# Optimization experiments

Hardware: AMD Instinct MI355X
Metric: run time of the kernel (lower is better)

## Reference

```python
import jax, jax.numpy as jnp
import numpy as np

B, S, H = 32, 2048, 1024

def setup_inputs() -> dict:
    key = jax.random.key(0)
    ks = jax.random.split(key, 6)
    sc = 0.02
    return {
        "decoder_state": jax.random.normal(ks[0], (B, H), jnp.float32),
        "encoder_output": jax.random.normal(ks[1], (B, S, H), jnp.float32),
        "coverage_vector": jax.random.uniform(ks[2], (B, S), jnp.float32),
        "Wh": jax.random.normal(ks[3], (H, H), jnp.float32) * sc,
        "bh": jnp.zeros((H,), jnp.float32),
        "Ws": jax.random.normal(ks[4], (H, H), jnp.float32) * sc,
        "bs": jnp.zeros((H,), jnp.float32),
        "V": jax.random.normal(ks[5], (H, 1), jnp.float32) * sc,
        "bv": jnp.zeros((1,), jnp.float32),
        "Wc": jax.random.normal(jax.random.fold_in(key, 7), (S, 1), jnp.float32) * sc,
        "bc": jnp.zeros((1,), jnp.float32),
    }

def reference(decoder_state, encoder_output, coverage_vector, Wh, bh, Ws, bs, V, bv, Wc, bc):
    # enc proj: (B,S,H); dec proj broadcast: (B,1,H)
    enc_p = jnp.einsum('bsh,hk->bsk', encoder_output, Wh) + bh
    dec_p = (decoder_state @ Ws + bs)[:, None, :]
    # Faithful to TF code: wc acts on expanded coverage (B,1,S) -> (B,1,1) scalar per batch
    cov_p = (coverage_vector @ Wc + bc)[:, None, :]          # (B,1,1)
    score = jnp.tanh(enc_p + dec_p + cov_p) @ V + bv          # (B,S,1)
    attention_weights = jax.nn.softmax(score, axis=1)        # (B,S,1)
    coverage_new = coverage_vector + attention_weights[..., 0]  # (B,S)
    context_vector = jnp.sum(attention_weights * encoder_output, axis=1)  # (B,H)
    return (context_vector, attention_weights, coverage_new)
```

## Files before the change

kernel.cpp:

```cpp
#include <hip/hip_runtime.h>

#define B_ 32
#define S_ 2048
#define H_ 1024

typedef __attribute__((ext_vector_type(8))) short short8;
typedef __attribute__((ext_vector_type(4))) float f32x4;
typedef __attribute__((ext_vector_type(4))) unsigned short u16x4;

__device__ __forceinline__ unsigned short f2bf(float f) {
    unsigned u = __builtin_bit_cast(unsigned, f);
    u += 0x7FFFu + ((u >> 16) & 1u);
    return (unsigned short)(u >> 16);
}
__device__ __forceinline__ unsigned pk2(float x, float y) {
    return (unsigned)f2bf(x) | ((unsigned)f2bf(y) << 16);
}
__device__ __forceinline__ float bf2f(unsigned short u) {
    unsigned x = ((unsigned)u) << 16;
    return __builtin_bit_cast(float, x);
}
__device__ __forceinline__ void gload16(const void* g, void* l) {
    __builtin_amdgcn_global_load_lds((const __attribute__((address_space(1))) void*)g,
                                     (__attribute__((address_space(3))) void*)l, 16, 0, 0);
}

#define WAITV(nstr) asm volatile("s_waitcnt vmcnt(" nstr ")" ::: "memory")

__global__ void k_cvt(const float* __restrict__ in, uint4* __restrict__ out, int ngroups) {
    int i = blockIdx.x * blockDim.x + threadIdx.x;
    int stride = gridDim.x * blockDim.x;
    for (; i < ngroups; i += stride) {
        const float4* p = (const float4*)in + (size_t)i * 2;
        float4 x = p[0], y = p[1];
        out[i] = make_uint4(pk2(x.x, x.y), pk2(x.z, x.w), pk2(y.x, y.y), pk2(y.z, y.w));
    }
}

__global__ void k_whT(const float* __restrict__ Wh, unsigned short* __restrict__ whT) {
    __shared__ float tile[64][65];
    int k0 = blockIdx.x * 64, n0 = blockIdx.y * 64;
    int tx = threadIdx.x, ty = threadIdx.y;
    #pragma unroll
    for (int i = 0; i < 16; ++i) {
        int r = ty + i * 4;
        tile[r][tx] = Wh[(size_t)(k0 + r) * H_ + n0 + tx];
    }
    __syncthreads();
    #pragma unroll
    for (int i = 0; i < 16; ++i) {
        int r = ty + i * 4;
        whT[(size_t)(n0 + r) * H_ + k0 + tx] = f2bf(tile[tx][r]);
    }
}

__global__ void k_decp(const float* __restrict__ ds, const float* __restrict__ Ws,
                       const float* __restrict__ bs, const float* __restrict__ bh,
                       float* __restrict__ decp) {
    int n = blockIdx.x * 256 + threadIdx.x;
    int b = blockIdx.y;
    float a0 = 0.f, a1 = 0.f, a2 = 0.f, a3 = 0.f;
    for (int h = 0; h < H_; h += 4) {
        a0 += ds[b * H_ + h + 0] * Ws[(size_t)(h + 0) * H_ + n];
        a1 += ds[b * H_ + h + 1] * Ws[(size_t)(h + 1) * H_ + n];
        a2 += ds[b * H_ + h + 2] * Ws[(size_t)(h + 2) * H_ + n];
        a3 += ds[b * H_ + h + 3] * Ws[(size_t)(h + 3) * H_ + n];
    }
    decp[b * H_ + n] = a0 + a1 + a2 + a3 + bs[n] + bh[n];
}

__global__ void k_covp(const float* __restrict__ cov, const float* __restrict__ Wc,
                       const float* __restrict__ bc, float* __restrict__ covp) {
    int b = blockIdx.x, t = threadIdx.x;
    float p = 0.f;
    for (int s = t; s < S_; s += 256) p += cov[b * S_ + s] * Wc[s];
    for (int off = 32; off; off >>= 1) p += __shfl_down(p, off);
    __shared__ float w[4];
    if ((t & 63) == 0) w[t >> 6] = p;
    __syncthreads();
    if (t == 0) covp[b] = w[0] + w[1] + w[2] + w[3] + bc[0];
}

__global__ __launch_bounds__(512, 2) void k_gemm_8w(
    const unsigned short* __restrict__ A, const unsigned short* __restrict__ Bm,
    const float* __restrict__ decp, const float* __restrict__ covp,
    const float* __restrict__ V, float* __restrict__ scores)
{
    __shared__ char lds[131072];

    int bid = blockIdx.x;
    int xcd = bid & 7, local = bid >> 3;
    int T = xcd * 128 + local;
    int tile_m = T >> 2, tile_n = T & 3;
    size_t row0 = (size_t)tile_m * 256;
    int n0 = tile_n * 256;

    int t = threadIdx.x, lane = t & 63, wid = t >> 6;
    int wm = wid >> 2, wn = wid & 3;
    int lrow = lane & 15, lk = (lane >> 4) * 8;

    const unsigned short* gA0 = A + (row0 + (size_t)(wid * 32) + lrow) * H_ + lk;
    const unsigned short* gA1 = gA0 + (size_t)16 * H_;
    const unsigned short* gB0 = Bm + ((size_t)(n0 + wid * 32 + lrow)) * H_ + lk;
    const unsigned short* gB1 = gB0 + (size_t)16 * H_;

    f32x4 acc[8][4] = {};

    auto stageA = [&](int kt) {
        char* lb = lds + (kt & 3) * 32768;
        gload16(gA0 + kt * 32, lb + (2 * wid) * 1024);
        gload16(gA1 + kt * 32, lb + (2 * wid + 1) * 1024);
    };
    auto stageB = [&](int kt) {
        char* lb = lds + (kt & 3) * 32768 + 16384;
        gload16(gB0 + kt * 32, lb + (2 * wid) * 1024);
        gload16(gB1 + kt * 32, lb + (2 * wid + 1) * 1024);
    };

    auto body = [&](int kt, bool pf) {
        const char* base = lds + (kt & 3) * 32768;
        short8 af[8], bf[4];
        #pragma unroll
        for (int m = 0; m < 8; ++m)
            af[m] = *(const short8*)(base + (wm * 8 + m) * 1024 + lane * 16);
        bf[0] = *(const short8*)(base + 16384 + (wn * 4 + 0) * 1024 + lane * 16);
        bf[1] = *(const short8*)(base + 16384 + (wn * 4 + 1) * 1024 + lane * 16);
        if (pf) stageA(kt + 3);
        __builtin_amdgcn_s_setprio(1);
        #pragma unroll
        for (int m = 0; m < 8; ++m) {
            acc[m][0] = __builtin_amdgcn_mfma_f32_16x16x32_bf16(af[m], bf[0], acc[m][0], 0, 0, 0);
            acc[m][1] = __builtin_amdgcn_mfma_f32_16x16x32_bf16(af[m], bf[1], acc[m][1], 0, 0, 0);
        }
        __builtin_amdgcn_s_setprio(0);
        bf[2] = *(const short8*)(base + 16384 + (wn * 4 + 2) * 1024 + lane * 16);
        bf[3] = *(const short8*)(base + 16384 + (wn * 4 + 3) * 1024 + lane * 16);
        if (pf) stageB(kt + 3);
        __builtin_amdgcn_s_setprio(1);
        #pragma unroll
        for (int m = 0; m < 8; ++m) {
            acc[m][2] = __builtin_amdgcn_mfma_f32_16x16x32_bf16(af[m], bf[2], acc[m][2], 0, 0, 0);
            acc[m][3] = __builtin_amdgcn_mfma_f32_16x16x32_bf16(af[m], bf[3], acc[m][3], 0, 0, 0);
        }
        __builtin_amdgcn_s_setprio(0);
    };

    stageA(0); stageB(0);
    stageA(1); stageB(1);
    stageA(2); stageB(2);

    for (int kt = 0; kt < 29; ++kt) {
        WAITV("8");
        __builtin_amdgcn_s_barrier();
        body(kt, true);
    }
    WAITV("8"); __builtin_amdgcn_s_barrier(); body(29, false);
    WAITV("4"); __builtin_amdgcn_s_barrier(); body(30, false);
    WAITV("0"); __builtin_amdgcn_s_barrier(); body(31, false);

    int colb = n0 + wn * 64 + (lane & 15);
    size_t rowg = row0 + (size_t)wm * 128;
    int b = (int)(row0 >> 11);
    float cb = covp[b];
    float vv[4], dp[4];
    #pragma unroll
    for (int n = 0; n < 4; ++n) {
        int c = colb + n * 16;
        vv[n] = V[c];
        dp[n] = decp[b * H_ + c] + cb;
    }
    #pragma unroll
    for (int m = 0; m < 8; ++m) {
        float rs[4] = {0.f, 0.f, 0.f, 0.f};
        #pragma unroll
        for (int n = 0; n < 4; ++n) {
            f32x4 Aq = acc[m][n];
            #pragma unroll
            for (int j = 0; j < 4; ++j) {
                float x = Aq[j] + dp[n];
                float e = __expf(2.f * x);
                float th = 1.f - 2.f / (e + 1.f);
                rs[j] += th * vv[n];
            }
        }
        #pragma unroll
        for (int off = 1; off < 16; off <<= 1) {
            #pragma unroll
            for (int j = 0; j < 4; ++j) rs[j] += __shfl_xor(rs[j], off);
        }
        if ((lane & 15) == 0) {
            size_t r = rowg + m * 16 + (lane >> 4) * 4;
            #pragma unroll
            for (int j = 0; j < 4; ++j) atomicAdd(&scores[r + j], rs[j]);
        }
    }
}

__device__ __forceinline__ void score_epilogue(
    f32x4 acc[4][4], int n0, int wm, int wn, int lane, size_t row0,
    const float* __restrict__ decp, const float* __restrict__ covp,
    const float* __restrict__ V, float* __restrict__ scores)
{
    int colb = n0 + wn * 64 + (lane & 15);
    size_t rowg = row0 + (size_t)wm * 64;
    int b = (int)(rowg >> 11);
    float cb = covp[b];
    float vv[4], dp[4];
    #pragma unroll
    for (int n = 0; n < 4; ++n) {
        int c = colb + n * 16;
        vv[n] = V[c];
        dp[n] = decp[b * H_ + c] + cb;
    }
    #pragma unroll
    for (int m = 0; m < 4; ++m) {
        float rs[4] = {0.f, 0.f, 0.f, 0.f};
        #pragma unroll
        for (int n = 0; n < 4; ++n) {
            f32x4 A = acc[m][n];
            #pragma unroll
            for (int j = 0; j < 4; ++j) {
                float x = A[j] + dp[n];
                float e = __expf(2.f * x);
                float th = 1.f - 2.f / (e + 1.f);
                rs[j] += th * vv[n];
            }
        }
        #pragma unroll
        for (int off = 1; off < 16; off <<= 1) {
            #pragma unroll
            for (int j = 0; j < 4; ++j) rs[j] += __shfl_xor(rs[j], off);
        }
        if ((lane & 15) == 0) {
            size_t r = rowg + m * 16 + (lane >> 4) * 4;
            #pragma unroll
            for (int j = 0; j < 4; ++j) atomicAdd(&scores[r + j], rs[j]);
        }
    }
}

__global__ __launch_bounds__(256, 2) void k_gemm_stage32(
    const float* __restrict__ enc, const unsigned short* __restrict__ whT,
    const float* __restrict__ decp, const float* __restrict__ covp,
    const float* __restrict__ V, float* __restrict__ scores)
{
    __shared__ uint4 lds[2][1024];
    int bid = blockIdx.x;
    int xcd = bid & 7, idx = bid >> 3;
    int tile_m = xcd * 64 + (idx >> 3);
    int tile_n = idx & 7;
    int t = threadIdx.x, lane = t & 63, wid = t >> 6;
    int wm = wid >> 1, wn = wid & 1;
    size_t row0 = (size_t)tile_m * 128;
    int n0 = tile_n * 128;
    int c0 = t, c1 = t + 256;
    int blk0 = c0 >> 6, l0 = c0 & 63, r0 = blk0 * 16 + (l0 & 15), ks0 = l0 >> 4;
    int blk1 = c1 >> 6, l1 = c1 & 63, r1 = blk1 * 16 + (l1 & 15), ks1 = l1 >> 4;
    const float* pa0 = enc + (row0 + r0) * H_ + ks0 * 8;
    const float* pa1 = enc + (row0 + r1) * H_ + ks1 * 8;
    const unsigned short* pb0 = whT + (size_t)(n0 + r0) * H_ + ks0 * 8;
    const unsigned short* pb1 = whT + (size_t)(n0 + r1) * H_ + ks1 * 8;
    f32x4 acc[4][4] = {};
    float4 a0x, a0y, a1x, a1y;
    uint4 b0, b1;
    auto LOAD = [&](int kt) {
        const float4* q0 = (const float4*)(pa0 + kt * 32);
        a0x = q0[0]; a0y = q0[1];
        const float4* q1 = (const float4*)(pa1 + kt * 32);
        a1x = q1[0]; a1y = q1[1];
        b0 = *(const uint4*)(pb0 + kt * 32);
        b1 = *(const uint4*)(pb1 + kt * 32);
    };
    auto WRITE = [&](int buf) {
        lds[buf][c0] = make_uint4(pk2(a0x.x, a0x.y), pk2(a0x.z, a0x.w),
                                  pk2(a0y.x, a0y.y), pk2(a0y.z, a0y.w));
        lds[buf][c1] = make_uint4(pk2(a1x.x, a1x.y), pk2(a1x.z, a1x.w),
                                  pk2(a1y.x, a1y.y), pk2(a1y.z, a1y.w));
        lds[buf][512 + c0] = b0;
        lds[buf][512 + c1] = b1;
    };
    LOAD(0); WRITE(0); __syncthreads();
    int cur = 0;
    for (int kt = 0; kt < 32; ++kt) {
        if (kt < 31) LOAD(kt + 1);
        const short8* LA = (const short8*)&lds[cur][0];
        const short8* LB = (const short8*)&lds[cur][512];
        short8 af[4], bf[4];
        #pragma unroll
        for (int m = 0; m < 4; ++m) af[m] = LA[(wm * 4 + m) * 64 + lane];
        #pragma unroll
        for (int n = 0; n < 4; ++n) bf[n] = LB[(wn * 4 + n) * 64 + lane];
        #pragma unroll
        for (int m = 0; m < 4; ++m)
            #pragma unroll
            for (int n = 0; n < 4; ++n)
                acc[m][n] = __builtin_amdgcn_mfma_f32_16x16x32_bf16(af[m], bf[n], acc[m][n], 0, 0, 0);
        if (kt < 31) WRITE(cur ^ 1);
        __syncthreads();
        cur ^= 1;
    }
    score_epilogue(acc, n0, wm, wn, lane, row0, decp, covp, V, scores);
}

__global__ void k_softmax(const float* __restrict__ scores, const float* __restrict__ cov,
                          float* __restrict__ out) {
    int b = blockIdx.x, t = threadIdx.x;
    float* attn = out + B_ * H_;
    float* covn = out + B_ * H_ + B_ * S_;
    float v[8];
    float mx = -1e30f;
    #pragma unroll
    for (int i = 0; i < 8; ++i) {
        v[i] = scores[b * S_ + i * 256 + t];
        mx = fmaxf(mx, v[i]);
    }
    for (int off = 32; off; off >>= 1) mx = fmaxf(mx, __shfl_xor(mx, off));
    __shared__ float wsm[4], wss[4];
    if ((t & 63) == 0) wsm[t >> 6] = mx;
    __syncthreads();
    mx = fmaxf(fmaxf(wsm[0], wsm[1]), fmaxf(wsm[2], wsm[3]));
    float sum = 0.f;
    #pragma unroll
    for (int i = 0; i < 8; ++i) { v[i] = __expf(v[i] - mx); sum += v[i]; }
    for (int off = 32; off; off >>= 1) sum += __shfl_xor(sum, off);
    if ((t & 63) == 0) wss[t >> 6] = sum;
    __syncthreads();
    sum = wss[0] + wss[1] + wss[2] + wss[3];
    float inv = 1.f / sum;
    #pragma unroll
    for (int i = 0; i < 8; ++i) {
        int s = i * 256 + t;
        float a = v[i] * inv;
        attn[b * S_ + s] = a;
        covn[b * S_ + s] = cov[b * S_ + s] + a;
    }
}

__global__ void k_context_bf(const unsigned short* __restrict__ encBF,
                             const float* __restrict__ attn, float* __restrict__ ctx) {
    int b = blockIdx.y, chunk = blockIdx.x;
    int t = threadIdx.x;
    __shared__ float sa[128];
    int s0 = chunk * 128;
    if (t < 128) sa[t] = attn[b * S_ + s0 + t];
    __syncthreads();
    float4 acc = {0.f, 0.f, 0.f, 0.f};
    const unsigned short* e = encBF + ((size_t)(b * S_ + s0)) * H_ + t * 4;
    #pragma unroll 4
    for (int s = 0; s < 128; ++s) {
        u16x4 x = *(const u16x4*)(e + (size_t)s * H_);
        float a = sa[s];
        acc.x += a * bf2f(x[0]); acc.y += a * bf2f(x[1]);
        acc.z += a * bf2f(x[2]); acc.w += a * bf2f(x[3]);
    }
    float* c = ctx + b * H_ + t * 4;
    atomicAdd(c + 0, acc.x); atomicAdd(c + 1, acc.y);
    atomicAdd(c + 2, acc.z); atomicAdd(c + 3, acc.w);
}

__global__ void k_context_f32(const float* __restrict__ enc, const float* __restrict__ attn,
                              float* __restrict__ ctx) {
    int b = blockIdx.y, chunk = blockIdx.x;
    int t = threadIdx.x;
    __shared__ float sa[128];
    int s0 = chunk * 128;
    if (t < 128) sa[t] = attn[b * S_ + s0 + t];
    __syncthreads();
    float4 acc = {0.f, 0.f, 0.f, 0.f};
    const float4* e = (const float4*)(enc + ((size_t)b * S_ + s0) * H_) + t;
    #pragma unroll 4
    for (int s = 0; s < 128; ++s) {
        float4 x = e[(size_t)s * (H_ / 4)];
        float a = sa[s];
        acc.x += a * x.x; acc.y += a * x.y; acc.z += a * x.z; acc.w += a * x.w;
    }
    float* c = ctx + b * H_ + t * 4;
    atomicAdd(c + 0, acc.x); atomicAdd(c + 1, acc.y);
    atomicAdd(c + 2, acc.z); atomicAdd(c + 3, acc.w);
}

extern "C" void kernel_launch(void* const* d_in, const int* in_sizes, int n_in,
                              void* d_out, int out_size, void* d_ws, size_t ws_size,
                              hipStream_t stream) {
    (void)in_sizes; (void)n_in; (void)out_size;
    const float* ds  = (const float*)d_in[0];
    const float* enc = (const float*)d_in[1];
    const float* cov = (const float*)d_in[2];
    const float* Wh  = (const float*)d_in[3];
    const float* bh  = (const float*)d_in[4];
    const float* Ws  = (const float*)d_in[5];
    const float* bs  = (const float*)d_in[6];
    const float* V   = (const float*)d_in[7];
    const float* Wc  = (const float*)d_in[9];
    const float* bc  = (const float*)d_in[10];
    float* out = (float*)d_out;

    float* ws_scores = (float*)d_ws;
    float* ws_decp   = ws_scores + B_ * S_;
    float* ws_covp   = ws_decp + B_ * H_;
    unsigned short* ws_whT = (unsigned short*)(ws_covp + 64);
    unsigned short* ws_encBF = ws_whT + (size_t)H_ * H_;
    const size_t need_full = ((char*)(ws_encBF + (size_t)B_ * S_ * H_)) - (char*)d_ws;

    hipMemsetAsync(ws_scores, 0, B_ * S_ * sizeof(float), stream);
    hipMemsetAsync(out, 0, B_ * H_ * sizeof(float), stream);

    k_whT<<<dim3(16, 16), dim3(64, 4), 0, stream>>>(Wh, ws_whT);
    k_decp<<<dim3(4, 32), 256, 0, stream>>>(ds, Ws, bs, bh, ws_decp);
    k_covp<<<32, 256, 0, stream>>>(cov, Wc, bc, ws_covp);

    if (ws_size >= need_full) {
        k_cvt<<<2048, 256, 0, stream>>>(enc, (uint4*)ws_encBF, (B_ * S_ * H_) / 8);
        k_gemm_8w<<<1024, 512, 0, stream>>>(ws_encBF, ws_whT, ws_decp, ws_covp, V, ws_scores);
        k_softmax<<<32, 256, 0, stream>>>(ws_scores, cov, out);
        k_context_bf<<<dim3(16, 32), 256, 0, stream>>>(ws_encBF, out + B_ * H_, out);
    } else {
        k_gemm_stage32<<<4096, 256, 0, stream>>>(enc, ws_whT, ws_decp, ws_covp, V, ws_scores);
        k_softmax<<<32, 256, 0, stream>>>(ws_scores, cov, out);
        k_context_f32<<<dim3(16, 32), 256, 0, stream>>>(enc, out + B_ * H_, out);
    }
}
```

Measured before the change: 340.4 us.

## Use 4-wave GEMM with 128x128 per-wave tiles and triple-buffered LDS

Replaces the 8-wave 256x256 GEMM block with a 4-wave block where each wave computes a 128x128 sub-tile (8x8 MFMA accumulators), cutting LDS reads per MFMA. The pipeline changes from 4-stage to 3-stage buffering with prefetch distance 2, using 96KB LDS. The larger per-wave tile raises register pressure to 256 accumulator VGPRs and leaves one block per CU, which risks lower latency hiding and spills.

```diff
diff --git a/kernel.cpp b/kernel.cpp
--- a/kernel.cpp
+++ b/kernel.cpp
@@ -26,6 +26,7 @@
 }
 
 #define WAITV(nstr) asm volatile("s_waitcnt vmcnt(" nstr ")" ::: "memory")
+#define BAR() __builtin_amdgcn_s_barrier()
 
 __global__ void k_cvt(const float* __restrict__ in, uint4* __restrict__ out, int ngroups) {
     int i = blockIdx.x * blockDim.x + threadIdx.x;
@@ -81,12 +82,12 @@
     if (t == 0) covp[b] = w[0] + w[1] + w[2] + w[3] + bc[0];
 }
 
-__global__ __launch_bounds__(512, 2) void k_gemm_8w(
+__global__ __launch_bounds__(256, 1) void k_gemm_fat(
     const unsigned short* __restrict__ A, const unsigned short* __restrict__ Bm,
     const float* __restrict__ decp, const float* __restrict__ covp,
     const float* __restrict__ V, float* __restrict__ scores)
 {
-    __shared__ char lds[131072];
+    __shared__ char lds[98304];
 
     int bid = blockIdx.x;
     int xcd = bid & 7, local = bid >> 3;
@@ -96,75 +97,65 @@
     int n0 = tile_n * 256;
 
     int t = threadIdx.x, lane = t & 63, wid = t >> 6;
-    int wm = wid >> 2, wn = wid & 3;
+    int wm = wid >> 1, wn = wid & 1;
     int lrow = lane & 15, lk = (lane >> 4) * 8;
 
-    const unsigned short* gA0 = A + (row0 + (size_t)(wid * 32) + lrow) * H_ + lk;
-    const unsigned short* gA1 = gA0 + (size_t)16 * H_;
-    const unsigned short* gB0 = Bm + ((size_t)(n0 + wid * 32 + lrow)) * H_ + lk;
-    const unsigned short* gB1 = gB0 + (size_t)16 * H_;
-
-    f32x4 acc[8][4] = {};
-
-    auto stageA = [&](int kt) {
-        char* lb = lds + (kt & 3) * 32768;
-        gload16(gA0 + kt * 32, lb + (2 * wid) * 1024);
-        gload16(gA1 + kt * 32, lb + (2 * wid + 1) * 1024);
+    const unsigned short* gA[4];
+    const unsigned short* gB[4];
+    #pragma unroll
+    for (int c = 0; c < 4; ++c) {
+        gA[c] = A + (row0 + (size_t)((4 * wid + c) * 16) + lrow) * H_ + lk;
+        gB[c] = Bm + ((size_t)(n0 + (4 * wid + c) * 16 + lrow)) * H_ + lk;
+    }
+
+    f32x4 acc[8][8] = {};
+
+    auto stage = [&](int h, int slot) {
+        char* lb = lds + slot * 32768;
+        #pragma unroll
+        for (int c = 0; c < 4; ++c) {
+            gload16(gA[c] + h * 32, lb + (4 * wid + c) * 1024);
+            gload16(gB[c] + h * 32, lb + 16384 + (4 * wid + c) * 1024);
+        }
     };
-    auto stageB = [&](int kt) {
-        char* lb = lds + (kt & 3) * 32768 + 16384;
-        gload16(gB0 + kt * 32, lb + (2 * wid) * 1024);
-        gload16(gB1 + kt * 32, lb + (2 * wid + 1) * 1024);
-    };
-
-    auto body = [&](int kt, bool pf) {
-        const char* base = lds + (kt & 3) * 32768;
-        short8 af[8], bf[4];
+
+    int aoff = wm * 8 * 1024 + lane * 16;
+    int boff = 16384 + wn * 8 * 1024 + lane * 16;
+
+    auto body = [&](int h, int slot, int pslot, bool pf) {
+        const char* base = lds + slot * 32768;
+        short8 af[8], bf[8];
+        #pragma unroll
+        for (int m = 0; m < 8; ++m) af[m] = *(const short8*)(base + aoff + m * 1024);
+        #pragma unroll
+        for (int n = 0; n < 8; ++n) bf[n] = *(const short8*)(base + boff + n * 1024);
+        if (pf) stage(h + 2, pslot);
+        __builtin_amdgcn_s_setprio(1);
         #pragma unroll
         for (int m = 0; m < 8; ++m)
-            af[m] = *(const short8*)(base + (wm * 8 + m) * 1024 + lane * 16);
-        bf[0] = *(const short8*)(base + 16384 + (wn * 4 + 0) * 1024 + lane * 16);
-        bf[1] = *(const short8*)(base + 16384 + (wn * 4 + 1) * 1024 + lane * 16);
-        if (pf) stageA(kt + 3);
-        __builtin_amdgcn_s_setprio(1);
-        #pragma unroll
-        for (int m = 0; m < 8; ++m) {
-            acc[m][0] = __builtin_amdgcn_mfma_f32_16x16x32_bf16(af[m], bf[0], acc[m][0], 0, 0, 0);
-            acc[m][1] = __builtin_amdgcn_mfma_f32_16x16x32_bf16(af[m], bf[1], acc[m][1], 0, 0, 0);
-        }
-        __builtin_amdgcn_s_setprio(0);
-        bf[2] = *(const short8*)(base + 16384 + (wn * 4 + 2) * 1024 + lane * 16);
-        bf[3] = *(const short8*)(base + 16384 + (wn * 4 + 3) * 1024 + lane * 16);
-        if (pf) stageB(kt + 3);
-        __builtin_amdgcn_s_setprio(1);
-        #pragma unroll
-        for (int m = 0; m < 8; ++m) {
-            acc[m][2] = __builtin_amdgcn_mfma_f32_16x16x32_bf16(af[m], bf[2], acc[m][2], 0, 0, 0);
-            acc[m][3] = __builtin_amdgcn_mfma_f32_16x16x32_bf16(af[m], bf[3], acc[m][3], 0, 0, 0);
-        }
+            #pragma unroll
+            for (int n = 0; n < 8; ++n)
+                acc[m][n] = __builtin_amdgcn_mfma_f32_16x16x32_bf16(af[m], bf[n], acc[m][n], 0, 0, 0);
         __builtin_amdgcn_s_setprio(0);
     };
 
-    stageA(0); stageB(0);
-    stageA(1); stageB(1);
-    stageA(2); stageB(2);
-
-    for (int kt = 0; kt < 29; ++kt) {
-        WAITV("8");
-        __builtin_amdgcn_s_barrier();
-        body(kt, true);
-    }
-    WAITV("8"); __builtin_amdgcn_s_barrier(); body(29, false);
-    WAITV("4"); __builtin_amdgcn_s_barrier(); body(30, false);
-    WAITV("0"); __builtin_amdgcn_s_barrier(); body(31, false);
-
-    int colb = n0 + wn * 64 + (lane & 15);
+    stage(0, 0); stage(1, 1);
+
+    for (int h = 0; h < 30; h += 3) {
+        WAITV("8"); BAR(); body(h + 0, 0, 2, true);
+        WAITV("8"); BAR(); body(h + 1, 1, 0, true);
+        WAITV("8"); BAR(); body(h + 2, 2, 1, true);
+    }
+    WAITV("8"); BAR(); body(30, 0, 2, false);
+    WAITV("0"); BAR(); body(31, 1, 0, false);
+
+    int colb = n0 + wn * 128 + (lane & 15);
     size_t rowg = row0 + (size_t)wm * 128;
     int b = (int)(row0 >> 11);
     float cb = covp[b];
-    float vv[4], dp[4];
-    #pragma unroll
-    for (int n = 0; n < 4; ++n) {
+    float vv[8], dp[8];
+    #pragma unroll
+    for (int n = 0; n < 8; ++n) {
         int c = colb + n * 16;
         vv[n] = V[c];
         dp[n] = decp[b * H_ + c] + cb;
@@ -173,7 +164,7 @@
     for (int m = 0; m < 8; ++m) {
         float rs[4] = {0.f, 0.f, 0.f, 0.f};
         #pragma unroll
-        for (int n = 0; n < 4; ++n) {
+        for (int n = 0; n < 8; ++n) {
             f32x4 Aq = acc[m][n];
             #pragma unroll
             for (int j = 0; j < 4; ++j) {
@@ -411,7 +402,7 @@
 
     if (ws_size >= need_full) {
         k_cvt<<<2048, 256, 0, stream>>>(enc, (uint4*)ws_encBF, (B_ * S_ * H_) / 8);
-        k_gemm_8w<<<1024, 512, 0, stream>>>(ws_encBF, ws_whT, ws_decp, ws_covp, V, ws_scores);
+        k_gemm_fat<<<1024, 256, 0, stream>>>(ws_encBF, ws_whT, ws_decp, ws_covp, V, ws_scores);
         k_softmax<<<32, 256, 0, stream>>>(ws_scores, cov, out);
         k_context_bf<<<dim3(16, 32), 256, 0, stream>>>(ws_encBF, out + B_ * H_, out);
     } else {
```

New measurement: 347.5 us. 2.1% more time.
